# Performance work log

Hardware: AMD Instinct MI355X
Metric: run time of the kernel (lower is better)

Reference implementation:

```python
import jax, jax.numpy as jnp
import numpy as np

BN_EPS = 1e-5


def setup_inputs() -> dict:
    key = jax.random.key(0)
    ks = jax.random.split(key, 9)
    b, c, h, w = 8, 256, 256, 25
    p2_r = jax.random.normal(ks[0], (b, c, h, w), dtype=jnp.float32)
    # message-passing conv weight; scaled so the 25-step recurrence stays bounded
    W_msg = jax.random.normal(ks[1], (256, 256, 1, 9), dtype=jnp.float32) * 0.02
    bn_gamma = jax.random.uniform(ks[2], (256,), dtype=jnp.float32, minval=0.5, maxval=1.5)
    bn_beta = jax.random.normal(ks[3], (256,), dtype=jnp.float32) * 0.1
    bn_mean = jax.random.normal(ks[4], (256,), dtype=jnp.float32) * 0.1
    bn_var = jax.random.uniform(ks[5], (256,), dtype=jnp.float32, minval=0.5, maxval=1.5)
    W_up2 = jax.random.normal(ks[6], (256, 256, 3, 3), dtype=jnp.float32) * (1.0 / np.sqrt(256 * 9))
    W_conv = jax.random.normal(ks[7], (1, 256, 1, 1), dtype=jnp.float32) * (1.0 / np.sqrt(256))
    W_conv2 = jax.random.normal(ks[8], (1, 25, 1, 1), dtype=jnp.float32) * (1.0 / np.sqrt(25))
    return {"p2_r": p2_r, "W_msg": W_msg, "bn_gamma": bn_gamma, "bn_beta": bn_beta,
            "bn_mean": bn_mean, "bn_var": bn_var, "W_up2": W_up2,
            "W_conv": W_conv, "W_conv2": W_conv2}


def r_scnn(x, Wc, reverse):
    # x: [b,c,h,w]. The (1,9) conv with padding (0,4) on width-1 slices only
    # touches the kernel's center tap -> per-step 256x256 matvec recurrence.
    xs = jnp.moveaxis(x, 3, 0)  # [w,b,c,h]
    if reverse:
        xs = xs[::-1]

    def step(carry, xi):
        new = xi + jax.nn.relu(jnp.einsum('oc,bch->boh', Wc, carry))
        return new, new

    _, rest = jax.lax.scan(step, xs[0], xs[1:])
    out = jnp.concatenate([xs[:1], rest], axis=0)[::-1]  # source reverses output order
    return jnp.moveaxis(out, 0, 3)  # [b,c,h,w]


def batchnorm(x, gamma, beta, mean, var):
    inv = gamma / jnp.sqrt(var + BN_EPS)
    return x * inv[None, :, None, None] + (beta - mean * inv)[None, :, None, None]


def upsample_h2(x):
    # bilinear, align_corners=True, size=(2H, W): only height doubles
    b, c, H, W = x.shape
    nh = 2 * H
    pos = jnp.arange(nh, dtype=jnp.float32) * ((H - 1) / (nh - 1))
    i0 = jnp.floor(pos).astype(jnp.int32)
    i1 = jnp.minimum(i0 + 1, H - 1)
    t = (pos - i0.astype(jnp.float32))[None, None, :, None]
    return x[:, :, i0, :] * (1.0 - t) + x[:, :, i1, :] * t


def reference(p2_r, W_msg, bn_gamma, bn_beta, bn_mean, bn_var, W_up2, W_conv, W_conv2):
    Wc = W_msg[:, :, 0, 4]  # effective center tap of the (1,9) conv
    x = r_scnn(p2_r, Wc, reverse=False)
    x = jax.nn.relu(batchnorm(x, bn_gamma, bn_beta, bn_mean, bn_var))
    x = r_scnn(x, Wc, reverse=True)
    x = jax.nn.relu(batchnorm(x, bn_gamma, bn_beta, bn_mean, bn_var))
    x = upsample_h2(x)  # [b,256,2h,w]
    x = jax.lax.conv_general_dilated(x, W_up2, (1, 1), ((1, 1), (1, 1)),
                                     dimension_numbers=('NCHW', 'OIHW', 'NCHW'))
    x = upsample_h2(x)  # [b,256,4h,w]
    x = jnp.einsum('oc,bchw->bohw', W_conv[:, :, 0, 0], x)  # 1x1 conv 256->1
    x = upsample_h2(x)  # [b,1,8h,w]
    x = jnp.swapaxes(x, 1, 3)  # [b,w,8h,1]
    x = jnp.einsum('oc,bchw->bohw', W_conv2[:, :, 0, 0], x)  # 1x1 conv 25->1
    return jax.nn.sigmoid(x)  # [b,1,8h,1]
```

## Files before the change

kernel.cpp:

```cpp
#include <hip/hip_runtime.h>
#include <math.h>


#define NC 8

typedef __attribute__((ext_vector_type(8))) short bf16x8;
typedef __attribute__((ext_vector_type(4))) float f32x4;

__device__ __forceinline__ float relu_(float v) { return fmaxf(v, 0.f); }

__device__ __forceinline__ short f2bf(float f) {
  union { float f; unsigned u; } v; v.f = f;
  unsigned r = (v.u + 0x7fffu + ((v.u >> 16) & 1u)) >> 16;
  return (short)r;
}
__device__ __forceinline__ float bf2f(short s) {
  union { unsigned u; float f; } v;
  v.u = ((unsigned)(unsigned short)s) << 16;
  return v.f;
}
__device__ __forceinline__ unsigned cvtpk(float lo, float hi) {
  unsigned r;
  asm("v_cvt_pk_bf16_f32 %0, %1, %2" : "=v"(r) : "v"(lo), "v"(hi));
  return r;
}
__device__ __forceinline__ float dpp_xor8(float v) {
  int r = __builtin_amdgcn_update_dpp(0, __float_as_int(v), 0x128, 0xf, 0xf, true);
  return __int_as_float(r);
}

__global__ __launch_bounds__(64) void k0_precompute(
    const float* __restrict__ Wmsg, const float* __restrict__ gamma,
    const float* __restrict__ beta, const float* __restrict__ mean,
    const float* __restrict__ var, const float* __restrict__ Wup2,
    const float* __restrict__ Wconv, const float* __restrict__ Wconv2,
    short* __restrict__ WcA, float* __restrict__ A, float* __restrict__ bnp)
{
  const int c = blockIdx.x;
  const int lane = threadIdx.x;

  for (int o = lane; o < 256; o += 64)
    WcA[o * 256 + c] = f2bf(Wmsg[(o * 256 + c) * 9 + 4]);

  const int gtid = c * 64 + lane;
  if (gtid < 256) {
    float inv = gamma[gtid] / sqrtf(var[gtid] + 1e-5f);
    bnp[gtid] = inv;
    bnp[256 + gtid] = beta[gtid] - mean[gtid] * inv;
  }

  float wacc[9];
#pragma unroll
  for (int q = 0; q < 9; ++q) wacc[q] = 0.f;
  for (int o = lane; o < 256; o += 64) {
    float cw = Wconv[o];
    const float* wp = Wup2 + (size_t)(o * 256 + c) * 9;
#pragma unroll
    for (int q = 0; q < 9; ++q) wacc[q] += cw * wp[q];
  }
#pragma unroll
  for (int q = 0; q < 9; ++q) {
    float v = wacc[q];
    v += __shfl_xor(v, 32, 64);
    v += __shfl_xor(v, 16, 64);
    v += __shfl_xor(v, 8, 64);
    v += __shfl_xor(v, 4, 64);
    v += __shfl_xor(v, 2, 64);
    v += __shfl_xor(v, 1, 64);
    wacc[q] = v;
  }
  if (lane == 0) {
    for (int dh = 0; dh < 3; ++dh)
      for (int j = 0; j < 25; ++j) {
        float a = 0.f;
        for (int dw = 0; dw < 3; ++dw) {
          int w = j + 1 - dw;
          if (w >= 0 && w < 25) a += wacc[dh * 3 + dw] * Wconv2[w];
        }
        A[(dh * 25 + j) * 256 + c] = a;
      }
  }
}

__global__ __launch_bounds__(256, 1) void k2_fused(
    const float* __restrict__ X,
    const short* __restrict__ WcA,
    const float* __restrict__ A,
    const float* __restrict__ bnp,
    float* __restrict__ S)
{
  __shared__ short xslab[25 * 8 * 256];
  __shared__ short yz[2][16 * 256];
  __shared__ float red[4][8][3];
  const int tid = threadIdx.x;
  const int wave = tid >> 6;
  const int lane = tid & 63;
  const int n = lane & 15;
  const int nr = n & 7;
  const int g = lane >> 4;
  const bool isz = (n >= 8);
  const int col0 = blockIdx.x * NC;
  const int b = col0 >> 8, h0 = col0 & 255;
  const int obase = wave * 64;
  char* xs = (char*)xslab;
  char* smem = (char*)yz;

  {
    const int L = lane;
    if (L < 50) {
      int base_[4], sx_[4];
#pragma unroll
      for (int e = 0; e < 4; ++e) {
        int f = 4 * L + e;
        int rn = f / 25, w = f - rn * 25;
        base_[e] = w * 4096 + rn * 512;
        sx_[e] = ((2 * rn + w) & 15) << 3;
      }
      const float* src0 = X + (size_t)(b * 256 + obase) * 6400 + h0 * 25 + 4 * L;
#pragma unroll 4
      for (int i = 0; i < 32; ++i) {
        float4 v0 = *(const float4*)(src0 + (size_t)(2 * i) * 6400);
        float4 v1 = *(const float4*)(src0 + (size_t)(2 * i + 1) * 6400);
        unsigned p[4] = {cvtpk(v0.x, v1.x), cvtpk(v0.y, v1.y),
                         cvtpk(v0.z, v1.z), cvtpk(v0.w, v1.w)};
        const int cb = 2 * obase + 4 * i;
#pragma unroll
        for (int e = 0; e < 4; ++e)
          *(unsigned*)(xs + base_[e] + (cb ^ sx_[e])) = p[e];
      }
    }
  }

  f32x4 inv[4], addv[4];
#pragma unroll
  for (int t = 0; t < 4; ++t) {
    inv[t] = *(const f32x4*)(bnp + obase + t * 16 + g * 4);
    addv[t] = *(const f32x4*)(bnp + 256 + obase + t * 16 + g * 4);
  }

  bf16x8 af[4][8];
#pragma unroll
  for (int t = 0; t < 4; ++t)
#pragma unroll
    for (int kk = 0; kk < 8; ++kk)
      af[t][kk] = *(const bf16x8*)(WcA + (obase + t * 16 + n) * 256 + kk * 32 + g * 8);

  const int swz = nr << 4;
  int woff[4], xb[4], roff[8];
#pragma unroll
  for (int t = 0; t < 4; ++t) {
    woff[t] = n * 512 + (((obase + t * 16 + g * 4) * 2) ^ swz);
    xb[t] = nr * 512 + 2 * (obase + t * 16 + g * 4);
  }
#pragma unroll
  for (int kk = 0; kk < 8; ++kk)
    roff[kk] = n * 512 + ((kk * 64 + g * 16) ^ swz);

  __syncthreads();

  {
    const int S0 = ((2 * nr) & 15) << 3;
#pragma unroll
    for (int t = 0; t < 4; ++t) {
      uint2 xq0 = *(const uint2*)(xs + (xb[t] ^ S0));
      if (!isz) {
        *(uint2*)(smem + woff[t]) = xq0;
      } else {
        float zr[4], t2r[4];
        float xv[4] = {bf2f((short)xq0.x), bf2f((short)(xq0.x >> 16)),
                       bf2f((short)xq0.y), bf2f((short)(xq0.y >> 16))};
#pragma unroll
        for (int r = 0; r < 4; ++r) {
          zr[r] = relu_(xv[r] * inv[t][r] + addv[t][r]);
          t2r[r] = relu_(zr[r] * inv[t][r] + addv[t][r]);
        }
        *(uint2*)(smem + woff[t]) = make_uint2(cvtpk(zr[0], zr[1]), cvtpk(zr[2], zr[3]));
        *(uint2*)(xs + (xb[t] ^ S0)) =
            make_uint2(cvtpk(t2r[0], t2r[1]), cvtpk(t2r[2], t2r[3]));
      }
    }
  }
  __syncthreads();

#pragma unroll 1
  for (int k = 1; k < 25; ++k) {
    const int cur = (k - 1) & 1, nxt = k & 1;
    const int Sk = ((2 * nr + k) & 15) << 3;
    const int kplane = k * 4096;

    uint2 xq[4];
#pragma unroll
    for (int t = 0; t < 4; ++t) xq[t] = make_uint2(0u, 0u);
    if (!isz) {
#pragma unroll
      for (int t = 0; t < 4; ++t)
        xq[t] = *(const uint2*)(xs + ((xb[t] + kplane) ^ Sk));
    }

    bf16x8 bfr[8];
#pragma unroll
    for (int kk = 0; kk < 8; ++kk)
      bfr[kk] = *(const bf16x8*)(smem + cur * 8192 + roff[kk]);

    f32x4 accA[4], accB[4];
#pragma unroll
    for (int t = 0; t < 4; ++t) {
      accA[t] = (f32x4){0.f, 0.f, 0.f, 0.f};
      accB[t] = (f32x4){0.f, 0.f, 0.f, 0.f};
    }
#pragma unroll
    for (int kk = 0; kk < 4; ++kk)
#pragma unroll
      for (int t = 0; t < 4; ++t)
        accA[t] = __builtin_amdgcn_mfma_f32_16x16x32_bf16(af[t][kk], bfr[kk], accA[t], 0, 0, 0);
#pragma unroll
    for (int kk = 4; kk < 8; ++kk)
#pragma unroll
      for (int t = 0; t < 4; ++t)
        accB[t] = __builtin_amdgcn_mfma_f32_16x16x32_bf16(af[t][kk], bfr[kk], accB[t], 0, 0, 0);

#pragma unroll
    for (int t = 0; t < 4; ++t) {
      f32x4 acc = accA[t] + accB[t];
      float xv[4];
      xv[0] = bf2f((short)xq[t].x);
      xv[1] = bf2f((short)(xq[t].x >> 16));
      xv[2] = bf2f((short)xq[t].y);
      xv[3] = bf2f((short)(xq[t].y >> 16));
      float sel[4], tt2[4];
#pragma unroll
      for (int r = 0; r < 4; ++r) {
        float cy = relu_(acc[r]);
        float ynew = xv[r] + cy;
        float t1 = relu_(ynew * inv[t][r] + addv[t][r]);
        float t1s = dpp_xor8(t1);
        float znew = t1s + cy;
        tt2[r] = relu_(znew * inv[t][r] + addv[t][r]);
        sel[r] = isz ? znew : ynew;
      }
      *(uint2*)(smem + nxt * 8192 + woff[t]) =
          make_uint2(cvtpk(sel[0], sel[1]), cvtpk(sel[2], sel[3]));
      if (isz)
        *(uint2*)(xs + ((xb[t] + kplane) ^ Sk)) =
            make_uint2(cvtpk(tt2[0], tt2[1]), cvtpk(tt2[2], tt2[3]));
    }
    __syncthreads();
  }

  {
    const int kb = (wave == 0) ? 0 : 1 + 6 * wave;
    const int ke = kb + (wave ? 6 : 7);
    float acc[8][3];
#pragma unroll
    for (int rn = 0; rn < 8; ++rn)
#pragma unroll
      for (int dh = 0; dh < 3; ++dh) acc[rn][dh] = 0.f;

#pragma unroll 1
    for (int k = kb; k < ke; ++k) {
      f32x4 a0 = *(const f32x4*)(A + (0 * 25 + 24 - k) * 256 + 4 * lane);
      f32x4 a1 = *(const f32x4*)(A + (1 * 25 + 24 - k) * 256 + 4 * lane);
      f32x4 a2 = *(const f32x4*)(A + (2 * 25 + 24 - k) * 256 + 4 * lane);
#pragma unroll
      for (int rn = 0; rn < 8; ++rn) {
        int Sp = ((2 * rn + k) & 15) << 3;
        uint2 q = *(const uint2*)(xs + ((k * 4096 + rn * 512 + 8 * lane) ^ Sp));
        float v0 = bf2f((short)q.x), v1 = bf2f((short)(q.x >> 16));
        float v2 = bf2f((short)q.y), v3 = bf2f((short)(q.y >> 16));
#pragma unroll
        for (int dh = 0; dh < 3; ++dh) {
          f32x4 a = dh == 0 ? a0 : (dh == 1 ? a1 : a2);
          float s = acc[rn][dh];
          s = fmaf(a[0], v0, s);
          s = fmaf(a[1], v1, s);
          s = fmaf(a[2], v2, s);
          s = fmaf(a[3], v3, s);
          acc[rn][dh] = s;
        }
      }
    }
#pragma unroll
    for (int rn = 0; rn < 8; ++rn)
#pragma unroll
      for (int dh = 0; dh < 3; ++dh) {
        float v = acc[rn][dh];
        v += __shfl_xor(v, 1);
        v += __shfl_xor(v, 2);
        v += __shfl_xor(v, 4);
        v += __shfl_xor(v, 8);
        v += __shfl_xor(v, 16);
        v += __shfl_xor(v, 32);
        if (lane == 0) red[wave][rn][dh] = v;
      }
  }
  __syncthreads();
  if (tid < 24) {
    int nn = tid / 3, dh = tid % 3;
    float v = red[0][nn][dh] + red[1][nn][dh] + red[2][nn][dh] + red[3][nn][dh];
    S[(size_t)(col0 + nn) * 3 + dh] = v;
  }
}

__global__ __launch_bounds__(256) void k3_outpre(
    const float* __restrict__ S, float* __restrict__ P)
{
  int idx = blockIdx.x * blockDim.x + threadIdx.x;
  if (idx >= 8 * 512) return;
  int b = idx >> 9, h = idx & 511;
  float acc = 0.f;
#pragma unroll
  for (int dh = 0; dh < 3; ++dh) {
    int hh = h + dh - 1;
    if (hh < 0 || hh >= 512) continue;
    float pos = hh * (255.0f / 511.0f);
    int i0 = (int)floorf(pos);
    int i1 = min(i0 + 1, 255);
    float t = pos - (float)i0;
    acc += (1.f - t) * S[(size_t)(b * 256 + i0) * 3 + dh]
         + t * S[(size_t)(b * 256 + i1) * 3 + dh];
  }
  P[idx] = acc;
}

__global__ __launch_bounds__(256) void k4_final(
    const float* __restrict__ P, float* __restrict__ out)
{
  int idx = blockIdx.x * blockDim.x + threadIdx.x;
  if (idx >= 8 * 2048) return;
  int b = idx >> 11, H = idx & 2047;
  const float* Pb = P + b * 512;

  float pos3 = H * (1023.0f / 2047.0f);
  int i3 = (int)floorf(pos3);
  int i3b = min(i3 + 1, 1023);
  float t3 = pos3 - (float)i3;

  float v[2];
#pragma unroll
  for (int q = 0; q < 2; ++q) {
    int i = q ? i3b : i3;
    float pos2 = i * (511.0f / 1023.0f);
    int i2 = (int)floorf(pos2);
    int i2b = min(i2 + 1, 511);
    float t2 = pos2 - (float)i2;
    v[q] = (1.f - t2) * Pb[i2] + t2 * Pb[i2b];
  }
  float val = (1.f - t3) * v[0] + t3 * v[1];
  out[idx] = 1.f / (1.f + expf(-val));
}

extern "C" void kernel_launch(void* const* d_in, const int* in_sizes, int n_in,
                              void* d_out, int out_size, void* d_ws, size_t ws_size,
                              hipStream_t stream) {
  (void)in_sizes; (void)n_in; (void)out_size; (void)ws_size;
  const float* p2r    = (const float*)d_in[0];
  const float* Wmsg   = (const float*)d_in[1];
  const float* gamma  = (const float*)d_in[2];
  const float* beta   = (const float*)d_in[3];
  const float* mean   = (const float*)d_in[4];
  const float* var    = (const float*)d_in[5];
  const float* Wup2   = (const float*)d_in[6];
  const float* Wconv  = (const float*)d_in[7];
  const float* Wconv2 = (const float*)d_in[8];
  float* out = (float*)d_out;

  float* ws = (float*)d_ws;
  size_t off = 0;
  short* WcA = (short*)(ws + off); off += 32768;
  float* Abuf = ws + off; off += 19200;
  float* bnp = ws + off;  off += 512;
  float* S = ws + off;    off += 6144;
  float* P = ws + off;    off += 4096;

  k0_precompute<<<256, 64, 0, stream>>>(Wmsg, gamma, beta, mean, var, Wup2,
                                        Wconv, Wconv2, WcA, Abuf, bnp);
  k2_fused<<<256, 256, 0, stream>>>(p2r, (const short*)WcA, Abuf, bnp, S);
  k3_outpre<<<16, 256, 0, stream>>>(S, P);
  k4_final<<<64, 256, 0, stream>>>(P, out);
}
```

Baseline: 58.63 us.

## Split input packing into separate kernel and run recurrence with 8 waves

The fp32-to-bf16 input transpose/pack moves into its own kernel that writes a swizzled bf16 slab to global workspace. The recurrence kernel then copies that slab into LDS and runs with 512 threads, each wave owning 32 output channels instead of 64. The next step's x values are prefetched before the barrier, and the epilogue is restructured so the DPP exchanges are batched. This halves per-wave MFMA work on the serial 24-step chain, at the cost of an extra kernel launch and a global round trip of the packed slab, plus more waves taking part in each barrier.

```diff
diff --git a/kernel.cpp b/kernel.cpp
--- a/kernel.cpp
+++ b/kernel.cpp
@@ -82,8 +82,51 @@
   }
 }
 
-__global__ __launch_bounds__(256, 1) void k2_fused(
-    const float* __restrict__ X,
+__global__ __launch_bounds__(256) void k2a_pack(
+    const float* __restrict__ X, char* __restrict__ xG)
+{
+  __shared__ short xslab[25 * 8 * 256];
+  const int tid = threadIdx.x;
+  const int wave = tid >> 6;
+  const int lane = tid & 63;
+  const int col0 = blockIdx.x * NC;
+  const int b = col0 >> 8, h0 = col0 & 255;
+  const int obase = wave * 64;
+  char* xs = (char*)xslab;
+
+  if (lane < 50) {
+    int base_[4], sx_[4];
+#pragma unroll
+    for (int e = 0; e < 4; ++e) {
+      int f = 4 * lane + e;
+      int rn = f / 25, w = f - rn * 25;
+      base_[e] = w * 4096 + rn * 512;
+      sx_[e] = ((2 * rn + w) & 15) << 3;
+    }
+    const float* src0 = X + (size_t)(b * 256 + obase) * 6400 + h0 * 25 + 4 * lane;
+#pragma unroll 4
+    for (int i = 0; i < 32; ++i) {
+      float4 v0 = *(const float4*)(src0 + (size_t)(2 * i) * 6400);
+      float4 v1 = *(const float4*)(src0 + (size_t)(2 * i + 1) * 6400);
+      unsigned p[4] = {cvtpk(v0.x, v1.x), cvtpk(v0.y, v1.y),
+                       cvtpk(v0.z, v1.z), cvtpk(v0.w, v1.w)};
+      const int cb = 2 * obase + 4 * i;
+#pragma unroll
+      for (int e = 0; e < 4; ++e)
+        *(unsigned*)(xs + base_[e] + (cb ^ sx_[e])) = p[e];
+    }
+  }
+  __syncthreads();
+
+  const uint4* src = (const uint4*)xs;
+  uint4* dst = (uint4*)(xG + (size_t)blockIdx.x * 102400);
+#pragma unroll
+  for (int i = 0; i < 25; ++i)
+    dst[i * 256 + tid] = src[i * 256 + tid];
+}
+
+__global__ __launch_bounds__(512, 1) void k2b_loop(
+    const char* __restrict__ xG,
     const short* __restrict__ WcA,
     const float* __restrict__ A,
     const float* __restrict__ bnp,
@@ -91,7 +134,7 @@
 {
   __shared__ short xslab[25 * 8 * 256];
   __shared__ short yz[2][16 * 256];
-  __shared__ float red[4][8][3];
+  __shared__ float red[8][8][3];
   const int tid = threadIdx.x;
   const int wave = tid >> 6;
   const int lane = tid & 63;
@@ -100,55 +143,34 @@
   const int g = lane >> 4;
   const bool isz = (n >= 8);
   const int col0 = blockIdx.x * NC;
-  const int b = col0 >> 8, h0 = col0 & 255;
-  const int obase = wave * 64;
+  const int obase = wave * 32;
   char* xs = (char*)xslab;
   char* smem = (char*)yz;
 
   {
-    const int L = lane;
-    if (L < 50) {
-      int base_[4], sx_[4];
-#pragma unroll
-      for (int e = 0; e < 4; ++e) {
-        int f = 4 * L + e;
-        int rn = f / 25, w = f - rn * 25;
-        base_[e] = w * 4096 + rn * 512;
-        sx_[e] = ((2 * rn + w) & 15) << 3;
-      }
-      const float* src0 = X + (size_t)(b * 256 + obase) * 6400 + h0 * 25 + 4 * L;
-#pragma unroll 4
-      for (int i = 0; i < 32; ++i) {
-        float4 v0 = *(const float4*)(src0 + (size_t)(2 * i) * 6400);
-        float4 v1 = *(const float4*)(src0 + (size_t)(2 * i + 1) * 6400);
-        unsigned p[4] = {cvtpk(v0.x, v1.x), cvtpk(v0.y, v1.y),
-                         cvtpk(v0.z, v1.z), cvtpk(v0.w, v1.w)};
-        const int cb = 2 * obase + 4 * i;
-#pragma unroll
-        for (int e = 0; e < 4; ++e)
-          *(unsigned*)(xs + base_[e] + (cb ^ sx_[e])) = p[e];
-      }
-    }
-  }
-
-  f32x4 inv[4], addv[4];
-#pragma unroll
-  for (int t = 0; t < 4; ++t) {
+    const uint4* gsrc = (const uint4*)(xG + (size_t)blockIdx.x * 102400);
+    uint4* ldst = (uint4*)xs;
+    for (int i = tid; i < 6400; i += 512) ldst[i] = gsrc[i];
+  }
+
+  f32x4 inv[2], addv[2];
+#pragma unroll
+  for (int t = 0; t < 2; ++t) {
     inv[t] = *(const f32x4*)(bnp + obase + t * 16 + g * 4);
     addv[t] = *(const f32x4*)(bnp + 256 + obase + t * 16 + g * 4);
   }
 
-  bf16x8 af[4][8];
-#pragma unroll
-  for (int t = 0; t < 4; ++t)
+  bf16x8 af[2][8];
+#pragma unroll
+  for (int t = 0; t < 2; ++t)
 #pragma unroll
     for (int kk = 0; kk < 8; ++kk)
       af[t][kk] = *(const bf16x8*)(WcA + (obase + t * 16 + n) * 256 + kk * 32 + g * 8);
 
   const int swz = nr << 4;
-  int woff[4], xb[4], roff[8];
-#pragma unroll
-  for (int t = 0; t < 4; ++t) {
+  int woff[2], xb[2], roff[8];
+#pragma unroll
+  for (int t = 0; t < 2; ++t) {
     woff[t] = n * 512 + (((obase + t * 16 + g * 4) * 2) ^ swz);
     xb[t] = nr * 512 + 2 * (obase + t * 16 + g * 4);
   }
@@ -161,7 +183,7 @@
   {
     const int S0 = ((2 * nr) & 15) << 3;
 #pragma unroll
-    for (int t = 0; t < 4; ++t) {
+    for (int t = 0; t < 2; ++t) {
       uint2 xq0 = *(const uint2*)(xs + (xb[t] ^ S0));
       if (!isz) {
         *(uint2*)(smem + woff[t]) = xq0;
@@ -180,76 +202,92 @@
       }
     }
   }
+
+  uint2 xq[2];
+  xq[0] = make_uint2(0u, 0u);
+  xq[1] = make_uint2(0u, 0u);
+  if (!isz) {
+    const int S1 = ((2 * nr + 1) & 15) << 3;
+#pragma unroll
+    for (int t = 0; t < 2; ++t)
+      xq[t] = *(const uint2*)(xs + ((xb[t] + 4096) ^ S1));
+  }
   __syncthreads();
 
 #pragma unroll 1
   for (int k = 1; k < 25; ++k) {
     const int cur = (k - 1) & 1, nxt = k & 1;
-    const int Sk = ((2 * nr + k) & 15) << 3;
-    const int kplane = k * 4096;
-
-    uint2 xq[4];
-#pragma unroll
-    for (int t = 0; t < 4; ++t) xq[t] = make_uint2(0u, 0u);
-    if (!isz) {
-#pragma unroll
-      for (int t = 0; t < 4; ++t)
-        xq[t] = *(const uint2*)(xs + ((xb[t] + kplane) ^ Sk));
-    }
 
     bf16x8 bfr[8];
 #pragma unroll
     for (int kk = 0; kk < 8; ++kk)
       bfr[kk] = *(const bf16x8*)(smem + cur * 8192 + roff[kk]);
 
-    f32x4 accA[4], accB[4];
-#pragma unroll
-    for (int t = 0; t < 4; ++t) {
+    f32x4 accA[2], accB[2];
+#pragma unroll
+    for (int t = 0; t < 2; ++t) {
       accA[t] = (f32x4){0.f, 0.f, 0.f, 0.f};
       accB[t] = (f32x4){0.f, 0.f, 0.f, 0.f};
     }
 #pragma unroll
     for (int kk = 0; kk < 4; ++kk)
 #pragma unroll
-      for (int t = 0; t < 4; ++t)
+      for (int t = 0; t < 2; ++t)
         accA[t] = __builtin_amdgcn_mfma_f32_16x16x32_bf16(af[t][kk], bfr[kk], accA[t], 0, 0, 0);
 #pragma unroll
     for (int kk = 4; kk < 8; ++kk)
 #pragma unroll
-      for (int t = 0; t < 4; ++t)
+      for (int t = 0; t < 2; ++t)
         accB[t] = __builtin_amdgcn_mfma_f32_16x16x32_bf16(af[t][kk], bfr[kk], accB[t], 0, 0, 0);
 
-#pragma unroll
-    for (int t = 0; t < 4; ++t) {
+    float cyv[2][4], ynv[2][4], t1v[2][4], t1s[2][4];
+#pragma unroll
+    for (int t = 0; t < 2; ++t) {
       f32x4 acc = accA[t] + accB[t];
       float xv[4];
       xv[0] = bf2f((short)xq[t].x);
       xv[1] = bf2f((short)(xq[t].x >> 16));
       xv[2] = bf2f((short)xq[t].y);
       xv[3] = bf2f((short)(xq[t].y >> 16));
+#pragma unroll
+      for (int r = 0; r < 4; ++r) {
+        cyv[t][r] = relu_(acc[r]);
+        ynv[t][r] = xv[r] + cyv[t][r];
+        t1v[t][r] = relu_(ynv[t][r] * inv[t][r] + addv[t][r]);
+      }
+    }
+#pragma unroll
+    for (int t = 0; t < 2; ++t)
+#pragma unroll
+      for (int r = 0; r < 4; ++r) t1s[t][r] = dpp_xor8(t1v[t][r]);
+#pragma unroll
+    for (int t = 0; t < 2; ++t) {
       float sel[4], tt2[4];
 #pragma unroll
       for (int r = 0; r < 4; ++r) {
-        float cy = relu_(acc[r]);
-        float ynew = xv[r] + cy;
-        float t1 = relu_(ynew * inv[t][r] + addv[t][r]);
-        float t1s = dpp_xor8(t1);
-        float znew = t1s + cy;
+        float znew = t1s[t][r] + cyv[t][r];
         tt2[r] = relu_(znew * inv[t][r] + addv[t][r]);
-        sel[r] = isz ? znew : ynew;
+        sel[r] = isz ? znew : ynv[t][r];
       }
       *(uint2*)(smem + nxt * 8192 + woff[t]) =
           make_uint2(cvtpk(sel[0], sel[1]), cvtpk(sel[2], sel[3]));
       if (isz)
-        *(uint2*)(xs + ((xb[t] + kplane) ^ Sk)) =
+        *(uint2*)(xs + ((xb[t] + k * 4096) ^ (((2 * nr + k) & 15) << 3))) =
             make_uint2(cvtpk(tt2[0], tt2[1]), cvtpk(tt2[2], tt2[3]));
     }
+
+    if (k < 24 && !isz) {
+      const int Sn = ((2 * nr + k + 1) & 15) << 3;
+#pragma unroll
+      for (int t = 0; t < 2; ++t)
+        xq[t] = *(const uint2*)(xs + ((xb[t] + (k + 1) * 4096) ^ Sn));
+    }
     __syncthreads();
   }
 
   {
-    const int kb = (wave == 0) ? 0 : 1 + 6 * wave;
-    const int ke = kb + (wave ? 6 : 7);
+    const int kb = (wave == 0) ? 0 : 4 + 3 * (wave - 1);
+    const int ke = kb + (wave ? 3 : 4);
     float acc[8][3];
 #pragma unroll
     for (int rn = 0; rn < 8; ++rn)
@@ -296,7 +334,9 @@
   __syncthreads();
   if (tid < 24) {
     int nn = tid / 3, dh = tid % 3;
-    float v = red[0][nn][dh] + red[1][nn][dh] + red[2][nn][dh] + red[3][nn][dh];
+    float v = 0.f;
+#pragma unroll
+    for (int ww = 0; ww < 8; ++ww) v += red[ww][nn][dh];
     S[(size_t)(col0 + nn) * 3 + dh] = v;
   }
 }
@@ -366,6 +406,7 @@
 
   float* ws = (float*)d_ws;
   size_t off = 0;
+  char* xG = (char*)(ws + off); off += 6553600;
   short* WcA = (short*)(ws + off); off += 32768;
   float* Abuf = ws + off; off += 19200;
   float* bnp = ws + off;  off += 512;
@@ -374,7 +415,8 @@
 
   k0_precompute<<<256, 64, 0, stream>>>(Wmsg, gamma, beta, mean, var, Wup2,
                                         Wconv, Wconv2, WcA, Abuf, bnp);
-  k2_fused<<<256, 256, 0, stream>>>(p2r, (const short*)WcA, Abuf, bnp, S);
+  k2a_pack<<<256, 256, 0, stream>>>(p2r, xG);
+  k2b_loop<<<256, 512, 0, stream>>>(xG, (const short*)WcA, Abuf, bnp, S);
   k3_outpre<<<16, 256, 0, stream>>>(S, P);
   k4_final<<<64, 256, 0, stream>>>(P, out);
 }
```

After: 63.37 us. 1.08x slower.
